# Kernel tuning notes

Hardware: AMD Instinct MI355X
Metric: run time of the kernel (lower is better)

Reference implementation:

```python
import jax, jax.numpy as jnp
import numpy as np

B, L, HID = 4, 4096, 1024
H, D = 16, 64  # num_heads, head_dim


def setup_inputs() -> dict:
    key = jax.random.key(0)
    ks = jax.random.split(key, 5)
    s = 1.0 / np.sqrt(HID)
    mk = lambda k: jax.random.uniform(k, (HID, HID), minval=-s, maxval=s, dtype=jnp.float32)
    return {
        "x": jax.random.normal(ks[0], (B, L, HID), dtype=jnp.float32),
        "Wq": mk(ks[1]), "bq": jnp.zeros((HID,), jnp.float32),
        "Wk": mk(ks[2]), "bk": jnp.zeros((HID,), jnp.float32),
        "Wv": mk(ks[3]), "bv": jnp.zeros((HID,), jnp.float32),
        "Wo": mk(ks[4]), "bo": jnp.zeros((HID,), jnp.float32),
    }


def reference(x, Wq, bq, Wk, bk, Wv, bv, Wo, bo):
    Bx, Lx, _ = x.shape
    # projections (weights stored [in, out])
    q = (x @ Wq + bq).reshape(Bx, Lx, H, D)
    k = (x @ Wk + bk).reshape(Bx, Lx, H, D)
    v = (x @ Wv + bv).reshape(Bx, Lx, H, D)
    # Single window (L <= window_size): torch matmul batches over (B, L) and
    # contracts head_dim -> per-token head-to-head scores [B, L, H, H].
    scores = jnp.einsum('blhd,bled->blhe', q, k) / np.sqrt(D).astype(np.float32)
    probs = jax.nn.softmax(scores, axis=-1)
    out = jnp.einsum('blhe,bled->blhd', probs, v).reshape(Bx, Lx, HID)
    return out @ Wo + bo
```

## Files before the change

### kernel.cpp

```cpp
#include <hip/hip_runtime.h>
#include <stdint.h>


typedef __attribute__((ext_vector_type(8))) short short8;
typedef __attribute__((ext_vector_type(4))) float floatx4;
typedef __attribute__((address_space(1))) unsigned int gu32;
typedef __attribute__((address_space(3))) unsigned int lu32;

#define HID 1024
#define MTOK 16384
#define WELEM (HID * HID)
#define XELEM (MTOK * HID)

__device__ __forceinline__ unsigned short f2bf(float f) {
  union { float f; uint32_t u; } v; v.f = f;
  uint32_t u = v.u;
  u += 0x7fffu + ((u >> 16) & 1u);
  return (unsigned short)(u >> 16);
}

__global__ __launch_bounds__(256) void cvt_x_kernel(const float* __restrict__ x,
                                                    unsigned short* __restrict__ xb) {
  const int idx = blockIdx.x * 256 + threadIdx.x;
  float4 v = ((const float4*)x)[idx];
  ushort4 o;
  o.x = f2bf(v.x); o.y = f2bf(v.y); o.z = f2bf(v.z); o.w = f2bf(v.w);
  ((ushort4*)xb)[idx] = o;
}

__global__ __launch_bounds__(256) void cvt_w_kernel(const float* __restrict__ W0,
                                                    const float* __restrict__ W1,
                                                    const float* __restrict__ W2,
                                                    const float* __restrict__ W3,
                                                    unsigned short* __restrict__ WT) {
  const float* W = (blockIdx.z == 0) ? W0 : (blockIdx.z == 1) ? W1
                   : (blockIdx.z == 2) ? W2 : W3;
  unsigned short* out = WT + (size_t)blockIdx.z * WELEM;
  __shared__ float tile[64][65];
  const int t = threadIdx.x;
  const int n0 = blockIdx.x * 64, k0 = blockIdx.y * 64;
#pragma unroll
  for (int i = 0; i < 4; i++) {
    const int row = i * 16 + (t >> 4);
    const int col = (t & 15) * 4;
    float4 v = *(const float4*)&W[(size_t)(k0 + row) * HID + n0 + col];
    tile[row][col] = v.x; tile[row][col + 1] = v.y;
    tile[row][col + 2] = v.z; tile[row][col + 3] = v.w;
  }
  __syncthreads();
#pragma unroll
  for (int i = 0; i < 4; i++) {
    const int n = i * 16 + (t >> 4);
    const int k = (t & 15) * 4;
    ushort4 o;
    o.x = f2bf(tile[k][n]);     o.y = f2bf(tile[k + 1][n]);
    o.z = f2bf(tile[k + 2][n]); o.w = f2bf(tile[k + 3][n]);
    *(ushort4*)&out[(size_t)(n0 + n) * HID + k0 + k] = o;
  }
}

template <bool QKV>
__global__ __launch_bounds__(256) void gemm_bt1d(
    const unsigned short* __restrict__ A,
    const unsigned short* __restrict__ BTb,
    const float* __restrict__ b0, const float* __restrict__ b1,
    const float* __restrict__ b2,
    void* __restrict__ Cv)
{
  const int i = blockIdx.x;
  const int xcd = i & 7;
  const int j = i >> 3;
  int mb, nb;
  if constexpr (QKV) {
    const int round = j / 192;
    const int jj = j - round * 192;
    nb = jj >> 3;
    mb = xcd * 8 + round * 64 + (jj & 7);
  } else {
    const int round = j >> 5;
    const int jj = j & 31;
    nb = jj >> 2;
    mb = xcd * 4 + round * 32 + (jj & 3);
  }
  const int z = QKV ? (nb >> 3) : 0;
  const int n0 = QKV ? ((nb & 7) * 128) : (nb * 128);
  const int m0 = mb * 128;
  const unsigned short* BT = BTb + (size_t)(QKV ? z : 3) * WELEM;
  const float* bias = QKV ? ((z == 0) ? b0 : ((z == 1) ? b1 : b2)) : b0;

  __shared__ unsigned short Als[128 * 32];
  __shared__ unsigned short Bls[128 * 32];

  const int t = threadIdx.x;
  const int wv = t >> 6;
  const int lane = t & 63;
  const int quad = lane >> 4;
  const int r16 = lane & 15;
  const int wr = wv >> 1, wc = wv & 1;

  floatx4 acc[4][4] = {};

  const int srow = t >> 2;
  const int scol = (t & 3) * 8;
  const unsigned short* Ag = A + (size_t)(m0 + srow) * HID + scol;
  const unsigned short* Bg = BT + (size_t)(n0 + srow) * HID + scol;
  unsigned short* Asl = Als + (wv * 16) * 32;
  unsigned short* Bsl = Bls + (wv * 16) * 32;

  for (int ko = 0; ko < HID; ko += 32) {
    __builtin_amdgcn_global_load_lds((const gu32*)(Ag + ko),            (lu32*)(Asl),            16, 0, 0);
    __builtin_amdgcn_global_load_lds((const gu32*)(Ag + 64 * HID + ko), (lu32*)(Asl + 64 * 32),  16, 0, 0);
    __builtin_amdgcn_global_load_lds((const gu32*)(Bg + ko),            (lu32*)(Bsl),            16, 0, 0);
    __builtin_amdgcn_global_load_lds((const gu32*)(Bg + 64 * HID + ko), (lu32*)(Bsl + 64 * 32),  16, 0, 0);
    __syncthreads();

    short8 a[4], b[4];
#pragma unroll
    for (int ii = 0; ii < 4; ii++)
      a[ii] = *(const short8*)(Als + (wr * 64 + ii * 16 + r16) * 32 + quad * 8);
#pragma unroll
    for (int jj = 0; jj < 4; jj++)
      b[jj] = *(const short8*)(Bls + (wc * 64 + jj * 16 + r16) * 32 + quad * 8);
#pragma unroll
    for (int ii = 0; ii < 4; ii++)
#pragma unroll
      for (int jj = 0; jj < 4; jj++)
        acc[ii][jj] = __builtin_amdgcn_mfma_f32_16x16x32_bf16(a[ii], b[jj], acc[ii][jj], 0, 0, 0);
    __syncthreads();
  }

#pragma unroll
  for (int jj = 0; jj < 4; jj++) {
    const int col = n0 + wc * 64 + jj * 16 + r16;
    const float bb = bias[col];
#pragma unroll
    for (int ii = 0; ii < 4; ii++) {
      const int row0 = m0 + wr * 64 + ii * 16 + quad * 4;
#pragma unroll
      for (int rr = 0; rr < 4; rr++) {
        const float val = acc[ii][jj][rr] + bb;
        if constexpr (QKV)
          ((unsigned short*)Cv)[(size_t)z * XELEM + (size_t)(row0 + rr) * HID + col] = f2bf(val);
        else
          ((float*)Cv)[(size_t)(row0 + rr) * HID + col] = val;
      }
    }
  }
}

__global__ __launch_bounds__(256) void attn_kernel(const unsigned short* qkv,
                                                   unsigned short* attn) {
  __shared__ unsigned short vls[4][1056];
  __shared__ unsigned short pls[4][16 * 24];

  const int t = threadIdx.x;
  const int wv = t >> 6, lane = t & 63;
  const int quad = lane >> 4, r16 = lane & 15;
  const size_t base = ((size_t)blockIdx.x * 4 + wv) * HID;
  const unsigned short* qp = qkv + base;
  const unsigned short* kp = qkv + (size_t)XELEM + base;
  const unsigned short* vp = qkv + 2 * (size_t)XELEM + base;

  __builtin_amdgcn_global_load_lds((const gu32*)(vp + lane * 8),       (lu32*)&vls[wv][0],   16, 0, 0);
  __builtin_amdgcn_global_load_lds((const gu32*)(vp + 512 + lane * 8), (lu32*)&vls[wv][528], 16, 0, 0);

  short8 qf0 = *(const short8*)(qp + r16 * 64 + quad * 8);
  short8 qf1 = *(const short8*)(qp + r16 * 64 + quad * 8 + 32);
  short8 kf0 = *(const short8*)(kp + r16 * 64 + quad * 8);
  short8 kf1 = *(const short8*)(kp + r16 * 64 + quad * 8 + 32);

  floatx4 sc = {0.f, 0.f, 0.f, 0.f};
  sc = __builtin_amdgcn_mfma_f32_16x16x32_bf16(qf0, kf0, sc, 0, 0, 0);
  sc = __builtin_amdgcn_mfma_f32_16x16x32_bf16(qf1, kf1, sc, 0, 0, 0);

#pragma unroll
  for (int rr = 0; rr < 4; rr++) {
    float s = sc[rr] * 0.125f;
    float m = s;
#pragma unroll
    for (int off = 1; off < 16; off <<= 1) m = fmaxf(m, __shfl_xor(m, off));
    float ex = __expf(s - m);
    float sum = ex;
#pragma unroll
    for (int off = 1; off < 16; off <<= 1) sum += __shfl_xor(sum, off);
    pls[wv][(quad * 4 + rr) * 24 + r16] = f2bf(ex / sum);
  }

  __syncthreads();

  const short8 zero8 = {0, 0, 0, 0, 0, 0, 0, 0};
  short8 af = zero8;
  short8 bf[4] = {zero8, zero8, zero8, zero8};
  if (quad < 2) {
    af = *(const short8*)&pls[wv][r16 * 24 + quad * 8];
#pragma unroll
    for (int c = 0; c < 4; c++)
#pragma unroll
      for (int jj = 0; jj < 8; jj++)
        bf[c][jj] = (short)vls[wv][quad * 528 + jj * 64 + c * 16 + r16];
  }

  floatx4 ov[4];
#pragma unroll
  for (int c = 0; c < 4; c++) {
    floatx4 z = {0.f, 0.f, 0.f, 0.f};
    ov[c] = __builtin_amdgcn_mfma_f32_16x16x32_bf16(af, bf[c], z, 0, 0, 0);
  }

#pragma unroll
  for (int rr = 0; rr < 4; rr++)
#pragma unroll
    for (int c = 0; c < 4; c++)
      attn[base + (size_t)(quad * 4 + rr) * 64 + c * 16 + r16] = f2bf(ov[c][rr]);
}

extern "C" void kernel_launch(void* const* d_in, const int* in_sizes, int n_in,
                              void* d_out, int out_size, void* d_ws, size_t ws_size,
                              hipStream_t stream) {
  const float* x  = (const float*)d_in[0];
  const float* Wq = (const float*)d_in[1];
  const float* bq = (const float*)d_in[2];
  const float* Wk = (const float*)d_in[3];
  const float* bk = (const float*)d_in[4];
  const float* Wv = (const float*)d_in[5];
  const float* bv = (const float*)d_in[6];
  const float* Wo = (const float*)d_in[7];
  const float* bo = (const float*)d_in[8];

  char* ws = (char*)d_ws;
  unsigned short* xb  = (unsigned short*)ws;
  unsigned short* wt  = (unsigned short*)(ws + (size_t)XELEM * 2);
  unsigned short* qkv = wt + 4 * (size_t)WELEM;

  cvt_x_kernel<<<XELEM / 1024, 256, 0, stream>>>(x, xb);
  cvt_w_kernel<<<dim3(16, 16, 4), 256, 0, stream>>>(Wq, Wk, Wv, Wo, wt);
  gemm_bt1d<true><<<3072, 256, 0, stream>>>(xb, wt, bq, bk, bv, (void*)qkv);
  attn_kernel<<<4096, 256, 0, stream>>>(qkv, qkv);
  gemm_bt1d<false><<<1024, 256, 0, stream>>>(qkv, wt, bo, bo, bo, d_out);
}
```

Baseline: 335.1 us.

## Replace GEMMs with 256x256-tile double-buffered pipelined MFMA kernel

Replaces the 128x128, single-buffered GEMM with a 256x256 tile kernel that uses 512 threads, a 64-wide K step, double-buffered LDS with swizzled layout, and staged global-to-LDS loads interleaved with four MFMA quadrants per iteration using s_setprio. It aims to raise arithmetic intensity and hide load latency behind compute, and to cut LDS bank conflicts. The cost is 128KB of LDS per block and fewer, larger blocks (768 and 256), which lowers occupancy and may leave CUs idle on the smaller output GEMM.

After: 302.5 us. -9.7%, faster.

```diff
diff --git a/kernel.cpp b/kernel.cpp
--- a/kernel.cpp
+++ b/kernel.cpp
@@ -11,6 +11,10 @@
 #define MTOK 16384
 #define WELEM (HID * HID)
 #define XELEM (MTOK * HID)
+
+#define SBAR() __builtin_amdgcn_s_barrier()
+#define WAITLGKM() do { asm volatile("s_waitcnt lgkmcnt(0)" ::: "memory"); \
+                        __builtin_amdgcn_sched_barrier(0); } while (0)
 
 __device__ __forceinline__ unsigned short f2bf(float f) {
   union { float f; uint32_t u; } v; v.f = f;
@@ -60,89 +64,164 @@
 }
 
 template <bool QKV>
-__global__ __launch_bounds__(256) void gemm_bt1d(
+__global__ __launch_bounds__(512, 2) void gemm256(
     const unsigned short* __restrict__ A,
     const unsigned short* __restrict__ BTb,
     const float* __restrict__ b0, const float* __restrict__ b1,
     const float* __restrict__ b2,
     void* __restrict__ Cv)
 {
-  const int i = blockIdx.x;
-  const int xcd = i & 7;
-  const int j = i >> 3;
-  int mb, nb;
-  if constexpr (QKV) {
-    const int round = j / 192;
-    const int jj = j - round * 192;
-    nb = jj >> 3;
-    mb = xcd * 8 + round * 64 + (jj & 7);
-  } else {
-    const int round = j >> 5;
-    const int jj = j & 31;
-    nb = jj >> 2;
-    mb = xcd * 4 + round * 32 + (jj & 3);
-  }
-  const int z = QKV ? (nb >> 3) : 0;
-  const int n0 = QKV ? ((nb & 7) * 128) : (nb * 128);
-  const int m0 = mb * 128;
-  const unsigned short* BT = BTb + (size_t)(QKV ? z : 3) * WELEM;
-  const float* bias = QKV ? ((z == 0) ? b0 : ((z == 1) ? b1 : b2)) : b0;
-
-  __shared__ unsigned short Als[128 * 32];
-  __shared__ unsigned short Bls[128 * 32];
-
-  const int t = threadIdx.x;
-  const int wv = t >> 6;
-  const int lane = t & 63;
-  const int quad = lane >> 4;
-  const int r16 = lane & 15;
-  const int wr = wv >> 1, wc = wv & 1;
-
-  floatx4 acc[4][4] = {};
-
-  const int srow = t >> 2;
-  const int scol = (t & 3) * 8;
-  const unsigned short* Ag = A + (size_t)(m0 + srow) * HID + scol;
+  __shared__ short8 smem_[131072 / 16];
+  char* smem = (char*)smem_;
+
+  const int bid = blockIdx.x;
+  const int xcd = bid & 7;
+  const int j = bid >> 3;
+  const int nb = j >> 3;
+  const int mb = xcd * 8 + (j & 7);
+  const int m0 = mb * 256;
+  const int n0 = nb * 256;
+
+  const unsigned short* BT = QKV ? BTb : (BTb + (size_t)3 * WELEM);
+
+  const int t_ = threadIdx.x;
+  const int wv = t_ >> 6, lane = t_ & 63;
+  const int quad = lane >> 4, r16 = lane & 15;
+  const int wm = wv >> 2, wn = wv & 3;
+
+  const int srow = wv * 16 + (lane >> 2);
+  const int scol = ((lane & 3) ^ ((lane >> 3) & 3)) * 8;
+  const unsigned short* Ag = A  + (size_t)(m0 + srow) * HID + scol;
   const unsigned short* Bg = BT + (size_t)(n0 + srow) * HID + scol;
-  unsigned short* Asl = Als + (wv * 16) * 32;
-  unsigned short* Bsl = Bls + (wv * 16) * 32;
-
-  for (int ko = 0; ko < HID; ko += 32) {
-    __builtin_amdgcn_global_load_lds((const gu32*)(Ag + ko),            (lu32*)(Asl),            16, 0, 0);
-    __builtin_amdgcn_global_load_lds((const gu32*)(Ag + 64 * HID + ko), (lu32*)(Asl + 64 * 32),  16, 0, 0);
-    __builtin_amdgcn_global_load_lds((const gu32*)(Bg + ko),            (lu32*)(Bsl),            16, 0, 0);
-    __builtin_amdgcn_global_load_lds((const gu32*)(Bg + 64 * HID + ko), (lu32*)(Bsl + 64 * 32),  16, 0, 0);
-    __syncthreads();
-
-    short8 a[4], b[4];
-#pragma unroll
-    for (int ii = 0; ii < 4; ii++)
-      a[ii] = *(const short8*)(Als + (wr * 64 + ii * 16 + r16) * 32 + quad * 8);
-#pragma unroll
-    for (int jj = 0; jj < 4; jj++)
-      b[jj] = *(const short8*)(Bls + (wc * 64 + jj * 16 + r16) * 32 + quad * 8);
-#pragma unroll
-    for (int ii = 0; ii < 4; ii++)
-#pragma unroll
-      for (int jj = 0; jj < 4; jj++)
-        acc[ii][jj] = __builtin_amdgcn_mfma_f32_16x16x32_bf16(a[ii], b[jj], acc[ii][jj], 0, 0, 0);
-    __syncthreads();
-  }
-
-#pragma unroll
-  for (int jj = 0; jj < 4; jj++) {
-    const int col = n0 + wc * 64 + jj * 16 + r16;
-    const float bb = bias[col];
-#pragma unroll
-    for (int ii = 0; ii < 4; ii++) {
-      const int row0 = m0 + wr * 64 + ii * 16 + quad * 4;
-#pragma unroll
-      for (int rr = 0; rr < 4; rr++) {
-        const float val = acc[ii][jj][rr] + bb;
-        if constexpr (QKV)
-          ((unsigned short*)Cv)[(size_t)z * XELEM + (size_t)(row0 + rr) * HID + col] = f2bf(val);
-        else
-          ((float*)Cv)[(size_t)(row0 + rr) * HID + col] = val;
+
+  const int qsw = (quad ^ ((r16 >> 1) & 3)) << 4;
+  const char* Ard = smem + wm * 16384 + r16 * 64 + qsw;
+  const char* Brd = smem + 32768 + (wn >> 1) * 16384 + ((wn & 1) * 64 + r16) * 64 + qsw;
+
+  floatx4 acc[8][4] = {};
+
+  auto stageA = [&](int h, int tt) {
+    const unsigned short* s = Ag + (size_t)h * 128 * HID + tt * 64;
+    char* d = smem + ((tt & 1) << 16) + h * 16384 + wv * 1024;
+    __builtin_amdgcn_global_load_lds((const gu32*)s,        (lu32*)d,          16, 0, 0);
+    __builtin_amdgcn_global_load_lds((const gu32*)(s + 32), (lu32*)(d + 8192), 16, 0, 0);
+  };
+  auto stageB = [&](int h, int tt) {
+    const unsigned short* s = Bg + (size_t)h * 128 * HID + tt * 64;
+    char* d = smem + ((tt & 1) << 16) + 32768 + h * 16384 + wv * 1024;
+    __builtin_amdgcn_global_load_lds((const gu32*)s,        (lu32*)d,          16, 0, 0);
+    __builtin_amdgcn_global_load_lds((const gu32*)(s + 32), (lu32*)(d + 8192), 16, 0, 0);
+  };
+
+  stageA(0, 0); stageA(1, 0); stageB(0, 0); stageB(1, 0);
+  stageB(0, 1); stageA(0, 1);
+  asm volatile("s_waitcnt vmcnt(4)" ::: "memory");
+  SBAR();
+
+  short8 a[4][2], b01[2][2], b23[2][2];
+  const int NT = HID / 64;
+
+  for (int t = 0; t < NT; ++t) {
+    const int bufb = (t & 1) << 16;
+
+#pragma unroll
+    for (int ks = 0; ks < 2; ++ks) {
+#pragma unroll
+      for (int mi = 0; mi < 4; ++mi)
+        a[mi][ks] = *(const short8*)(Ard + bufb + ks * 8192 + mi * 1024);
+#pragma unroll
+      for (int ni = 0; ni < 2; ++ni)
+        b01[ni][ks] = *(const short8*)(Brd + bufb + ks * 8192 + ni * 1024);
+    }
+    if (t + 1 < NT) stageA(1, t + 1);
+    SBAR(); WAITLGKM();
+    __builtin_amdgcn_s_setprio(1);
+#pragma unroll
+    for (int ks = 0; ks < 2; ++ks)
+#pragma unroll
+      for (int mi = 0; mi < 4; ++mi)
+#pragma unroll
+        for (int ni = 0; ni < 2; ++ni)
+          acc[mi][ni] = __builtin_amdgcn_mfma_f32_16x16x32_bf16(a[mi][ks], b01[ni][ks], acc[mi][ni], 0, 0, 0);
+    __builtin_amdgcn_s_setprio(0);
+    SBAR();
+
+#pragma unroll
+    for (int ks = 0; ks < 2; ++ks)
+#pragma unroll
+      for (int ni = 0; ni < 2; ++ni)
+        b23[ni][ks] = *(const short8*)(Brd + bufb + ks * 8192 + (2 + ni) * 1024);
+    if (t + 1 < NT) stageB(1, t + 1);
+    SBAR(); WAITLGKM();
+    __builtin_amdgcn_s_setprio(1);
+#pragma unroll
+    for (int ks = 0; ks < 2; ++ks)
+#pragma unroll
+      for (int mi = 0; mi < 4; ++mi)
+#pragma unroll
+        for (int ni = 0; ni < 2; ++ni)
+          acc[mi][2 + ni] = __builtin_amdgcn_mfma_f32_16x16x32_bf16(a[mi][ks], b23[ni][ks], acc[mi][2 + ni], 0, 0, 0);
+    __builtin_amdgcn_s_setprio(0);
+    SBAR();
+
+#pragma unroll
+    for (int ks = 0; ks < 2; ++ks) {
+#pragma unroll
+      for (int mi = 0; mi < 4; ++mi)
+        a[mi][ks] = *(const short8*)(Ard + bufb + ks * 8192 + (4 + mi) * 1024);
+#pragma unroll
+      for (int ni = 0; ni < 2; ++ni)
+        b01[ni][ks] = *(const short8*)(Brd + bufb + ks * 8192 + ni * 1024);
+    }
+    SBAR(); WAITLGKM();
+    __builtin_amdgcn_s_setprio(1);
+#pragma unroll
+    for (int ks = 0; ks < 2; ++ks)
+#pragma unroll
+      for (int mi = 0; mi < 4; ++mi)
+#pragma unroll
+        for (int ni = 0; ni < 2; ++ni)
+          acc[4 + mi][ni] = __builtin_amdgcn_mfma_f32_16x16x32_bf16(a[mi][ks], b01[ni][ks], acc[4 + mi][ni], 0, 0, 0);
+    __builtin_amdgcn_s_setprio(0);
+    SBAR();
+
+    if (t + 2 < NT) { stageB(0, t + 2); stageA(0, t + 2); }
+    SBAR();
+    __builtin_amdgcn_s_setprio(1);
+#pragma unroll
+    for (int ks = 0; ks < 2; ++ks)
+#pragma unroll
+      for (int mi = 0; mi < 4; ++mi)
+#pragma unroll
+        for (int ni = 0; ni < 2; ++ni)
+          acc[4 + mi][2 + ni] = __builtin_amdgcn_mfma_f32_16x16x32_bf16(a[mi][ks], b23[ni][ks], acc[4 + mi][2 + ni], 0, 0, 0);
+    __builtin_amdgcn_s_setprio(0);
+    if (t + 2 < NT)      { asm volatile("s_waitcnt vmcnt(4)" ::: "memory"); }
+    else if (t + 1 < NT) { asm volatile("s_waitcnt vmcnt(0)" ::: "memory"); }
+    SBAR();
+  }
+
+  const int cb = QKV ? (n0 & 1023) : n0;
+  const int zX = QKV ? (n0 >> 10) : 0;
+  const float* bias = QKV ? ((zX == 0) ? b0 : ((zX == 1) ? b1 : b2)) : b0;
+
+  float bvv[4];
+#pragma unroll
+  for (int ni = 0; ni < 4; ++ni) bvv[ni] = bias[cb + wn * 64 + ni * 16 + r16];
+
+  const int row0 = m0 + wm * 128 + quad * 4;
+  unsigned short* outb = (unsigned short*)Cv + (size_t)zX * XELEM;
+  float* outf = (float*)Cv;
+#pragma unroll
+  for (int mi = 0; mi < 8; ++mi) {
+#pragma unroll
+    for (int rr = 0; rr < 4; ++rr) {
+      const size_t roff = (size_t)(row0 + mi * 16 + rr) * HID + cb + wn * 64 + r16;
+#pragma unroll
+      for (int ni = 0; ni < 4; ++ni) {
+        const float val = acc[mi][ni][rr] + bvv[ni];
+        if constexpr (QKV) outb[roff + ni * 16] = f2bf(val);
+        else               outf[roff + ni * 16] = val;
       }
     }
   }
@@ -234,7 +313,7 @@
 
   cvt_x_kernel<<<XELEM / 1024, 256, 0, stream>>>(x, xb);
   cvt_w_kernel<<<dim3(16, 16, 4), 256, 0, stream>>>(Wq, Wk, Wv, Wo, wt);
-  gemm_bt1d<true><<<3072, 256, 0, stream>>>(xb, wt, bq, bk, bv, (void*)qkv);
+  gemm256<true><<<768, 512, 0, stream>>>(xb, wt, bq, bk, bv, (void*)qkv);
   attn_kernel<<<4096, 256, 0, stream>>>(qkv, qkv);
-  gemm_bt1d<false><<<1024, 256, 0, stream>>>(qkv, wt, bo, bo, bo, d_out);
-}
+  gemm256<false><<<256, 512, 0, stream>>>(qkv, wt, bo, bo, bo, d_out);
+}
```
